# Performance work log

Hardware: AMD Instinct MI355X
Metric: run time of the kernel (lower is better)

The kernel has to match this reference:

```python
import jax, jax.numpy as jnp
import numpy as np
from jax import lax

BS, TLEN, N, S = 256, 3, 90, 65
CHEV, TF, NC = 45, 10, 2
FEAT = (N - 2) * (CHEV - 2)          # 88*43 = 3784
FLAT = TLEN * FEAT                    # 11352
BN_EPS = 1e-5
DN = ('NCHW', 'OIHW', 'NCHW')


def _pearson_cheb_adj(x):
    """x: (B, N, S) -> (B, 3, N, N): [T0=I, T1=L_tilde, T2=2*L*T1-T0 (elementwise)]."""
    xc = x - x.mean(axis=2, keepdims=True)
    y = xc / (jnp.linalg.norm(xc, axis=2, keepdims=True) + 1e-6)
    corr = jnp.einsum('bns,bms->bnm', y, y)
    W = (corr + 1.0) * 0.5
    I = jnp.eye(N, dtype=W.dtype)
    L = I[None] * jnp.sum(W, axis=2)[:, :, None] - W          # D - W, symmetric PSD
    # original uses torch.linalg.eig + .item() (detached); eigvalsh is equivalent for symmetric L
    lam = lax.stop_gradient(jnp.max(jnp.abs(jnp.linalg.eigvalsh(L)), axis=1))
    Lt = 2.0 * L / lam[:, None, None] - I
    T0 = jnp.broadcast_to(I, Lt.shape)
    T2 = 2.0 * Lt * Lt - T0                                   # elementwise, per cheb_polynomial
    return jnp.stack([T0, Lt, T2], axis=1)


def _bn_eval(x, g, b):
    # eval-mode BatchNorm1d with running_mean=0, running_var=1
    return x * (g / jnp.sqrt(jnp.float32(1.0 + BN_EPS))) + b


def setup_inputs() -> dict:
    key = jax.random.key(0)
    ks = jax.random.split(key, 12)
    rn = lambda k, shp, s: jax.random.normal(k, shp, dtype=jnp.float32) * s
    return {
        'fdata':   rn(ks[0], (BS, TLEN, N, S), 1.0),
        'un_w':    rn(ks[1], (N * S, 1), 0.01),
        'un_b':    jnp.zeros((1,), jnp.float32),
        'theta':   rn(ks[2], (3, S, CHEV), 0.05),
        'tconv_w': rn(ks[3], (TF, TLEN, 3, 3), 0.1),
        'tconv_b': jnp.zeros((TF,), jnp.float32),
        'oconv_w': rn(ks[4], (1, TF, 1, 1), 0.1),
        'oconv_b': jnp.zeros((1,), jnp.float32),
        'l1_w':    rn(ks[5], (FLAT, 1024), 0.01),
        'l1_b':    jnp.zeros((1024,), jnp.float32),
        'bn1_g':   jnp.ones((1024,), jnp.float32),
        'bn1_b':   jnp.zeros((1024,), jnp.float32),
        'l2_w':    rn(ks[6], (1024, 256), 0.03),
        'l2_b':    jnp.zeros((256,), jnp.float32),
        'bn2_g':   jnp.ones((256,), jnp.float32),
        'bn2_b':   jnp.zeros((256,), jnp.float32),
        'l3_w':    rn(ks[7], (256, NC), 0.06),
        'l3_b':    jnp.zeros((NC,), jnp.float32),
    }


def reference(fdata, un_w, un_b, theta, tconv_w, tconv_b, oconv_w, oconv_b,
              l1_w, l1_b, bn1_g, bn1_b, l2_w, l2_b, bn2_g, bn2_b, l3_w, l3_b):
    bs, tlen, n, s = fdata.shape
    fp = jnp.transpose(fdata, (1, 0, 2, 3))                    # (tlen, bs, N, S)

    # Uncertainty head (replicates original's tlen-major reshape then bs-major view)
    u = fp.reshape(tlen * bs, n * s) @ un_w + un_b
    cs = jax.nn.sigmoid(u.reshape(bs, tlen, 1))                # (bs, tlen, 1)

    # per-(sample,timestep) pearson Laplacian + Chebyshev basis
    adj = _pearson_cheb_adj(fp.reshape(tlen * bs, n, s))       # (tlen*bs, 3, N, N)
    adj = adj.reshape(tlen, bs, 3, n, n)

    def st_block(adj_t):                                       # adj_t: (bs, 3, N, N)
        h = jax.nn.relu(jnp.einsum('bknm,btms,kso->btno', adj_t, fdata, theta))  # (bs,tlen,N,45)
        c = lax.conv_general_dilated(h, tconv_w, (1, 1), 'VALID', dimension_numbers=DN)
        c = jax.nn.relu(c + tconv_b[None, :, None, None])      # (bs,10,88,43)
        o = lax.conv_general_dilated(c, oconv_w, (1, 1), 'VALID', dimension_numbers=DN)
        return o + oconv_b[None, :, None, None]                # (bs,1,88,43)

    block = jax.vmap(st_block)(adj)                            # (tlen, bs, 1, 88, 43)
    block = block.squeeze(2).reshape(tlen, bs, -1)             # (tlen, bs, 3784)
    block = jnp.transpose(block, (1, 0, 2))                    # (bs, tlen, 3784)

    # sum_s cs[b,s] * block[b,t,f]  ==  block * cs.sum(axis=1) (original broadcast quirk)
    final = block * jnp.sum(cs, axis=1)[:, :, None]            # (bs, tlen, 3784)

    x = final.reshape(bs, -1)                                  # (bs, 11352)
    x = _bn_eval(x @ l1_w + l1_b, bn1_g, bn1_b)
    x = _bn_eval(x @ l2_w + l2_b, bn2_g, bn2_b)
    return jax.nn.softmax(x @ l3_w + l3_b, axis=1)
```

## Files before the change

kernel.cpp:

```cpp
#include <hip/hip_runtime.h>
#include <math.h>

#define TPB 256

constexpr int BSZ = 256, TL = 3, NV = 90, SV = 65, CH = 45;
constexpr int NS = NV*SV;
constexpr int NP = TL*BSZ;
constexpr int NM = NV*NV;
constexpr int CCOL = TL*CH;
constexpr int ZLD = 136;
constexpr int CONV_H = 88, CONV_W = 43, FEAT = CONV_H*CONV_W;
constexpr int FLATD = TL*FEAT;

constexpr size_t OFF_CSUM = 0;
constexpr size_t OFF_LAM  = 256;
constexpr size_t OFF_BEFF = 1024;
constexpr size_t OFF_M    = 1056;
constexpr size_t OFF_MA   = 3104;
constexpr size_t OFF_WEFF = 5152;
constexpr size_t OFF_L    = 32768;
constexpr size_t OFF_Z    = 6291456;
constexpr size_t OFF_X    = 15728640;

__global__ __launch_bounds__(TPB) void k_corr(const float* __restrict__ fdata,
    const float* __restrict__ unw, const float* __restrict__ unb,
    float* __restrict__ Lout, float* __restrict__ csum)
{
    __shared__ float yT[65*96];
    __shared__ float Dl[NV], Wd[NV];
    __shared__ float red[TPB];

    const int q = blockIdx.x, tid = threadIdx.x;
    const int t = q >> 8, b = q & 255;
    const float* xp = fdata + ((size_t)b*TL + t)*NS;
    const int wave = tid >> 6, lane = tid & 63;

    if (tid < NV) Dl[tid] = 0.f;

    float up = 0.f;
    for (int n = wave; n < NV; n += 4) {
        const float* row = xp + n*SV;
        float va = row[lane];
        float vb = (lane == 0) ? row[64] : 0.f;
        up += va*unw[n*SV + lane];
        if (lane == 0) up += vb*unw[n*SV + 64];
        float s1 = va + vb, s2 = va*va + vb*vb;
        #pragma unroll
        for (int o = 1; o < 64; o <<= 1) { s1 += __shfl_xor(s1, o); s2 += __shfl_xor(s2, o); }
        float mean = s1 / SV;
        float var  = s2 - SV*mean*mean;
        float inv  = 1.f / (sqrtf(fmaxf(var, 0.f)) + 1e-6f);
        yT[lane*96 + (((n >> 2) + lane) % 24)*4 + (n & 3)] = (va - mean)*inv;
        if (lane == 0)
            yT[64*96 + (((n >> 2) + 64) % 24)*4 + (n & 3)] = (vb - mean)*inv;
    }
    red[tid] = up; __syncthreads();
    if (tid < 128) red[tid] += red[tid+128]; __syncthreads();
    if (tid < 64)  red[tid] += red[tid+64];  __syncthreads();
    if (tid < 64) {
        float x = red[tid];
        #pragma unroll
        for (int o = 32; o >= 1; o >>= 1) x += __shfl_down(x, o);
        if (tid == 0) {
            float u = x + unb[0];
            atomicAdd(csum + (q/3), 1.f/(1.f + expf(-u)));
        }
    }
    __syncthreads();

    float* Lq = Lout + (size_t)q*NM;
    for (int tile = tid; tile < 529; tile += TPB) {
        int tr = tile / 23, tc = tile - tr*23;
        int n0 = 4*tr, m0 = 4*tc;
        int ca = tr, cb = tc;
        float acc[4][4] = {};
        for (int s = 0; s < SV; ++s) {
            const float* base = &yT[s*96];
            float4 a4 = *(const float4*)(base + 4*ca);
            float4 b4 = *(const float4*)(base + 4*cb);
            float av[4] = {a4.x, a4.y, a4.z, a4.w};
            float bv[4] = {b4.x, b4.y, b4.z, b4.w};
            #pragma unroll
            for (int i = 0; i < 4; ++i)
                #pragma unroll
                for (int j = 0; j < 4; ++j) acc[i][j] += av[i]*bv[j];
            if (++ca == 24) ca = 0;
            if (++cb == 24) cb = 0;
        }
        #pragma unroll
        for (int i = 0; i < 4; ++i) {
            int n = n0 + i;
            if (n >= NV) break;
            float rsum = 0.f;
            #pragma unroll
            for (int j = 0; j < 4; ++j) {
                int m = m0 + j;
                if (m < NV) {
                    float w = (acc[i][j] + 1.f)*0.5f;
                    rsum += w;
                    if (n != m) Lq[n*NV + m] = -w;
                    else        Wd[n] = w;
                }
            }
            atomicAdd(&Dl[n], rsum);
        }
    }
    __syncthreads();
    if (tid < NV) Lq[tid*(NV+1)] = Dl[tid] - Wd[tid];
}

__global__ __launch_bounds__(TPB) void k_eig(const float* __restrict__ L,
                                             float* __restrict__ lamOut)
{
    __shared__ float vbuf[4][2][92];
    const int tid = threadIdx.x, w = tid >> 6, lane = tid & 63;
    const int q = blockIdx.x*4 + w;
    const float* Lq = L + (size_t)q*NM;

    float LA[92], LB[92];
    {
        const float2* ra = (const float2*)(Lq + lane*NV);
        #pragma unroll
        for (int j = 0; j < 45; ++j) { float2 x = ra[j]; LA[2*j] = x.x; LA[2*j+1] = x.y; }
        LA[90] = 0.f; LA[91] = 0.f;
        if (lane < 26) {
            const float2* rb = (const float2*)(Lq + (64 + lane)*NV);
            #pragma unroll
            for (int j = 0; j < 45; ++j) { float2 x = rb[j]; LB[2*j] = x.x; LB[2*j+1] = x.y; }
        } else {
            #pragma unroll
            for (int j = 0; j < 90; ++j) LB[j] = 0.f;
        }
        LB[90] = 0.f; LB[91] = 0.f;
    }
    if (lane < 2) { vbuf[w][0][90+lane] = 0.f; vbuf[w][1][90+lane] = 0.f; }

    float vA = sinf(1.3f*lane + 0.5f) + 0.05f;
    float vB = (lane < 26) ? (sinf(1.3f*(64 + lane) + 0.5f) + 0.05f) : 0.f;
    int cur = 0;
    float wA = 0.f, wB = 0.f;

    auto share = [&]() {
        vbuf[w][cur][lane] = vA;
        if (lane < 26) vbuf[w][cur][64 + lane] = vB;
        __syncthreads();
    };
    auto matvec = [&](float sigma) {
        const float4* v4 = (const float4*)&vbuf[w][cur][0];
        float p0=0.f,p1=0.f,p2=0.f,p3=0.f, r0=0.f,r1=0.f,r2=0.f,r3=0.f;
        #pragma unroll
        for (int j = 0; j < 23; ++j) {
            float4 x = v4[j];
            p0 += LA[4*j]*x.x;   p1 += LA[4*j+1]*x.y;
            p2 += LA[4*j+2]*x.z; p3 += LA[4*j+3]*x.w;
            r0 += LB[4*j]*x.x;   r1 += LB[4*j+1]*x.y;
            r2 += LB[4*j+2]*x.z; r3 += LB[4*j+3]*x.w;
        }
        wA = (p0+p1) + (p2+p3) - sigma*vA;
        wB = (r0+r1) + (r2+r3) - sigma*vB;
        cur ^= 1;
    };
    auto renorm = [&]() {
        float t1 = vA + ((lane < 26) ? vB : 0.f);
        float t2 = vA*vA + ((lane < 26) ? vB*vB : 0.f);
        #pragma unroll
        for (int o = 1; o < 64; o <<= 1) { t1 += __shfl_xor(t1, o); t2 += __shfl_xor(t2, o); }
        float mean = t1*(1.f/90.f);
        float ns   = t2 - 90.f*mean*mean;
        float rn   = rsqrtf(fmaxf(ns, 1e-30f));
        vA = (vA - mean)*rn; vB = (vB - mean)*rn;
    };
    auto dotvw = [&]() {
        float d = vA*wA + ((lane < 26) ? vB*wB : 0.f);
        #pragma unroll
        for (int o = 1; o < 64; o <<= 1) d += __shfl_xor(d, o);
        return d;
    };

    for (int it = 0; it < 8; ++it) { share(); matvec(0.f); vA = wA; vB = wB; }
    renorm();
    share(); matvec(0.f);
    float ray = dotvw();
    float sigma = 0.45f*ray;
    vA = wA - sigma*vA; vB = wB - sigma*vB;
    for (int it = 0; it < 87; ++it) {
        if ((it & 7) == 7) renorm();
        share(); matvec(sigma); vA = wA; vB = wB;
    }
    renorm();
    share(); matvec(0.f);
    float lam = dotvw();
    if (lane == 0) lamOut[q] = lam;
}

__global__ __launch_bounds__(TPB) void k_Z(const float* __restrict__ fdata,
                                           const float* __restrict__ theta,
                                           float* __restrict__ Z)
{
    __shared__ float fl[NV][69];
    __shared__ float thl[3][SV][48];

    const int g = blockIdx.x, tid = threadIdx.x;
    const int b = g/3, tp = g - 3*b;
    const float* fp = fdata + ((size_t)b*TL + tp)*NS;

    for (int idx = tid; idx < NS; idx += TPB) {
        int m = idx / SV, s = idx - m*SV;
        fl[m][s] = fp[idx];
    }
    for (int idx = tid; idx < 3*SV*48; idx += TPB) {
        int k = idx / (SV*48), rr = idx - k*(SV*48);
        int s = rr / 48, o = rr - s*48;
        thl[k][s][o] = (o < CH) ? theta[(k*SV + s)*CH + o] : 0.f;
    }
    __syncthreads();

    for (int tile = tid; tile < 414; tile += TPB) {
        int mt = tile / 18, ct = tile - mt*18;
        int k = ct / 6, ot = ct - 6*k;
        int m0 = 4*mt, o0 = 8*ot;
        float acc[4][8] = {};
        for (int s = 0; s < SV; ++s) {
            float a0 = fl[m0][s], a1 = fl[m0+1][s], a2 = fl[m0+2][s], a3 = fl[m0+3][s];
            float4 t0 = *(const float4*)&thl[k][s][o0];
            float4 t1 = *(const float4*)&thl[k][s][o0+4];
            float tv[8] = {t0.x,t0.y,t0.z,t0.w,t1.x,t1.y,t1.z,t1.w};
            #pragma unroll
            for (int j = 0; j < 8; ++j) {
                acc[0][j] += a0*tv[j]; acc[1][j] += a1*tv[j];
                acc[2][j] += a2*tv[j]; acc[3][j] += a3*tv[j];
            }
        }
        #pragma unroll
        for (int i = 0; i < 4; ++i) {
            int m = m0 + i; if (m >= NV) break;
            float* zp = Z + ((size_t)(k*BSZ + b)*NV + m)*ZLD + tp*CH;
            #pragma unroll
            for (int j = 0; j < 8; ++j) {
                int o = o0 + j;
                if (o < CH) zp[o] = acc[i][j];
            }
        }
    }
    if (tp == 2) {
        for (int idx = tid; idx < 3*NV; idx += TPB) {
            int k = idx / NV, m = idx - k*NV;
            Z[((size_t)(k*BSZ + b)*NV + m)*ZLD + 135] = 0.f;
        }
    }
}

__global__ __launch_bounds__(TPB) void k_hc(const float* __restrict__ L,
    const float* __restrict__ lam, const float* __restrict__ Z,
    const float* __restrict__ tw, const float* __restrict__ tb,
    const float* __restrict__ ow, const float* __restrict__ ob,
    const float* __restrict__ csum, float* __restrict__ X)
{
    __shared__ float smem[12160];
    const int q = blockIdx.x, tid = threadIdx.x;
    const int t = q >> 8, b = q & 255;
    const float il2 = 2.0f / lam[q];

    for (int idx = tid; idx < NM; idx += TPB) {
        int i = idx / NV, j = idx - i*NV;
        smem[i*92 + j] = il2 * L[(size_t)q*NM + idx] - ((i == j) ? 1.f : 0.f);
    }
    __syncthreads();

    float acc[6][8];
    const int tn = tid / 17, tc = tid - tn*17;
    const int n0 = 6*tn, c0 = 8*tc;
    const bool act = (tid < 255);
    if (act) {
        #pragma unroll
        for (int i = 0; i < 6; ++i)
            #pragma unroll
            for (int j = 0; j < 8; ++j) acc[i][j] = 0.f;
        const float* z1p = Z + ((size_t)(BSZ + b)*NV)*ZLD + c0;
        const float* z2p = Z + ((size_t)(2*BSZ + b)*NV)*ZLD + c0;
        for (int m = 0; m < NV; ++m) {
            const float* ar = &smem[m*92 + n0];
            float2 a01 = *(const float2*)(ar);
            float2 a23 = *(const float2*)(ar + 2);
            float2 a45 = *(const float2*)(ar + 4);
            float av[6] = {a01.x, a01.y, a23.x, a23.y, a45.x, a45.y};
            const float4* z1r = (const float4*)(z1p + (size_t)m*ZLD);
            const float4* z2r = (const float4*)(z2p + (size_t)m*ZLD);
            float4 z1a = z1r[0], z1b = z1r[1];
            float4 z2a = z2r[0], z2b = z2r[1];
            float zv1[8] = {z1a.x,z1a.y,z1a.z,z1a.w,z1b.x,z1b.y,z1b.z,z1b.w};
            float zv2[8] = {z2a.x,z2a.y,z2a.z,z2a.w,z2b.x,z2b.y,z2b.z,z2b.w};
            #pragma unroll
            for (int i = 0; i < 6; ++i) {
                float a = av[i], bb = 2.f*a*a;
                #pragma unroll
                for (int j = 0; j < 8; ++j) acc[i][j] += a*zv1[j] + bb*zv2[j];
            }
        }
    }
    __syncthreads();

    float (*hl)[NV][CH] = (float (*)[NV][CH])smem;
    if (act) {
        const float* z0p = Z + ((size_t)b*NV)*ZLD;
        const float* z2p = Z + ((size_t)(2*BSZ + b)*NV)*ZLD;
        #pragma unroll
        for (int i = 0; i < 6; ++i) {
            int n = n0 + i;
            const float4* z0r = (const float4*)(z0p + (size_t)n*ZLD + c0);
            const float4* z2r = (const float4*)(z2p + (size_t)n*ZLD + c0);
            float4 z0a = z0r[0], z0b = z0r[1];
            float4 w2a = z2r[0], w2b = z2r[1];
            float zv0[8] = {z0a.x,z0a.y,z0a.z,z0a.w,z0b.x,z0b.y,z0b.z,z0b.w};
            float zv2[8] = {w2a.x,w2a.y,w2a.z,w2a.w,w2b.x,w2b.y,w2b.z,w2b.w};
            #pragma unroll
            for (int j = 0; j < 8; ++j) {
                int c = c0 + j;
                if (c < CCOL) {
                    float v = fmaxf(acc[i][j] + zv0[j] - zv2[j], 0.f);
                    hl[c/CH][n][c - (c/CH)*CH] = v;
                }
            }
        }
    }
    __syncthreads();

    const float cs  = csum[b];
    const float obv = ob[0];
    float* Xo = X + (size_t)b*FLATD + (size_t)t*FEAT;
    for (int g = tid; g < 88*11; g += TPB) {
        int i = g / 11, jg = g - (g/11)*11, j0 = 4*jg;
        float cf[10][4];
        #pragma unroll
        for (int f = 0; f < 10; ++f) {
            float bv = tb[f];
            cf[f][0] = bv; cf[f][1] = bv; cf[f][2] = bv; cf[f][3] = bv;
        }
        #pragma unroll
        for (int tp = 0; tp < 3; ++tp)
            #pragma unroll
            for (int di = 0; di < 3; ++di) {
                const float* hr = &hl[tp][i + di][j0];
                float w0 = hr[0], w1 = hr[1], w2 = hr[2],
                      w3 = hr[3], w4 = hr[4], w5 = hr[5];
                #pragma unroll
                for (int f = 0; f < 10; ++f) {
                    const float* twp = tw + ((f*TL + tp)*3 + di)*3;
                    float t0 = twp[0], t1 = twp[1], t2 = twp[2];
                    cf[f][0] += w0*t0 + w1*t1 + w2*t2;
                    cf[f][1] += w1*t0 + w2*t1 + w3*t2;
                    cf[f][2] += w2*t0 + w3*t1 + w4*t2;
                    cf[f][3] += w3*t0 + w4*t1 + w5*t2;
                }
            }
        float a0 = 0.f, a1 = 0.f, a2 = 0.f, a3 = 0.f;
        #pragma unroll
        for (int f = 0; f < 10; ++f) {
            float o = ow[f];
            a0 += fmaxf(cf[f][0], 0.f)*o; a1 += fmaxf(cf[f][1], 0.f)*o;
            a2 += fmaxf(cf[f][2], 0.f)*o; a3 += fmaxf(cf[f][3], 0.f)*o;
        }
        int pixb = i*CONV_W + j0;
        Xo[pixb] = (a0 + obv)*cs;
        if (j0 + 1 < CONV_W) Xo[pixb+1] = (a1 + obv)*cs;
        if (j0 + 2 < CONV_W) Xo[pixb+2] = (a2 + obv)*cs;
        if (j0 + 3 < CONV_W) Xo[pixb+3] = (a3 + obv)*cs;
    }
}

__global__ void k_eff1(const float* __restrict__ W2, const float* __restrict__ g2,
                       const float* __restrict__ W3, const float* __restrict__ g1,
                       float* __restrict__ M, float* __restrict__ Ma)
{
    int gid = blockIdx.x*TPB + threadIdx.x;
    if (gid >= 2048) return;
    int i = gid >> 1, c = gid & 1;
    const float rs = rsqrtf(1.f + 1e-5f);
    float acc = 0.f;
    for (int j = 0; j < 256; ++j) acc += W2[i*256 + j]*(g2[j]*rs)*W3[j*2 + c];
    M[gid]  = acc;
    Ma[gid] = acc*(g1[i]*rs);
}

__global__ void k_effb(const float* __restrict__ M, const float* __restrict__ W3,
                       const float* __restrict__ b1, const float* __restrict__ bb1, const float* __restrict__ g1,
                       const float* __restrict__ b2, const float* __restrict__ bb2, const float* __restrict__ g2,
                       const float* __restrict__ b3, float* __restrict__ beff)
{
    __shared__ float r0[TPB], r1[TPB];
    int tid = threadIdx.x;
    const float rs = rsqrtf(1.f + 1e-5f);
    float a0 = 0.f, a1 = 0.f;
    for (int i = tid; i < 1024; i += TPB) {
        float wv = b1[i]*(g1[i]*rs) + bb1[i];
        a0 += wv*M[2*i]; a1 += wv*M[2*i+1];
    }
    for (int j = tid; j < 256; j += TPB) {
        float wv = b2[j]*(g2[j]*rs) + bb2[j];
        a0 += wv*W3[2*j]; a1 += wv*W3[2*j+1];
    }
    r0[tid] = a0; r1[tid] = a1; __syncthreads();
    if (tid < 128) { r0[tid] += r0[tid+128]; r1[tid] += r1[tid+128]; } __syncthreads();
    if (tid < 64)  { r0[tid] += r0[tid+64];  r1[tid] += r1[tid+64];  } __syncthreads();
    if (tid < 64) {
        float x0 = r0[tid], x1 = r1[tid];
        #pragma unroll
        for (int o = 32; o >= 1; o >>= 1) { x0 += __shfl_down(x0, o); x1 += __shfl_down(x1, o); }
        if (tid == 0) { beff[0] = x0 + b3[0]; beff[1] = x1 + b3[1]; }
    }
}

__global__ void k_eff2(const float* __restrict__ W1, const float* __restrict__ Ma,
                       float* __restrict__ Weff)
{
    int tid = threadIdx.x;
    int r = blockIdx.x*4 + (tid >> 6);
    int lane = tid & 63;
    if (r >= FLATD) return;
    const float* wrow = W1 + (size_t)r*1024;
    float a0 = 0.f, a1 = 0.f;
    for (int i = lane; i < 1024; i += 64) {
        float w = wrow[i];
        a0 += w*Ma[2*i]; a1 += w*Ma[2*i+1];
    }
    #pragma unroll
    for (int o = 32; o >= 1; o >>= 1) { a0 += __shfl_down(a0, o); a1 += __shfl_down(a1, o); }
    if (lane == 0) { Weff[2*r] = a0; Weff[2*r+1] = a1; }
}

__global__ void k_logits(const float* __restrict__ x, const float* __restrict__ Weff,
                         const float* __restrict__ beff, float* __restrict__ out)
{
    __shared__ float r0[TPB], r1[TPB];
    int b = blockIdx.x, tid = threadIdx.x;
    const float* xr = x + (size_t)b*FLATD;
    float a0 = 0.f, a1 = 0.f;
    for (int i = tid; i < FLATD; i += TPB) {
        float v = xr[i];
        a0 += v*Weff[2*i]; a1 += v*Weff[2*i+1];
    }
    r0[tid] = a0; r1[tid] = a1; __syncthreads();
    if (tid < 128) { r0[tid] += r0[tid+128]; r1[tid] += r1[tid+128]; } __syncthreads();
    if (tid < 64)  { r0[tid] += r0[tid+64];  r1[tid] += r1[tid+64];  } __syncthreads();
    if (tid < 64) {
        float x0 = r0[tid], x1 = r1[tid];
        #pragma unroll
        for (int o = 32; o >= 1; o >>= 1) { x0 += __shfl_down(x0, o); x1 += __shfl_down(x1, o); }
        if (tid == 0) {
            float l0 = x0 + beff[0], l1 = x1 + beff[1];
            float mx = fmaxf(l0, l1);
            float e0 = expf(l0 - mx), e1 = expf(l1 - mx);
            float s = e0 + e1;
            out[2*b]     = e0/s;
            out[2*b + 1] = e1/s;
        }
    }
}

extern "C" void kernel_launch(void* const* d_in, const int* in_sizes, int n_in,
                              void* d_out, int out_size, void* d_ws, size_t ws_size,
                              hipStream_t stream)
{
    const float* fdata = (const float*)d_in[0];
    const float* un_w  = (const float*)d_in[1];
    const float* un_b  = (const float*)d_in[2];
    const float* theta = (const float*)d_in[3];
    const float* tcw   = (const float*)d_in[4];
    const float* tcb   = (const float*)d_in[5];
    const float* ocw   = (const float*)d_in[6];
    const float* ocb   = (const float*)d_in[7];
    const float* l1w   = (const float*)d_in[8];
    const float* l1b   = (const float*)d_in[9];
    const float* bn1g  = (const float*)d_in[10];
    const float* bn1b  = (const float*)d_in[11];
    const float* l2w   = (const float*)d_in[12];
    const float* l2b   = (const float*)d_in[13];
    const float* bn2g  = (const float*)d_in[14];
    const float* bn2b  = (const float*)d_in[15];
    const float* l3w   = (const float*)d_in[16];
    const float* l3b   = (const float*)d_in[17];

    float* ws   = (float*)d_ws;
    float* csum = ws + OFF_CSUM;
    float* lam  = ws + OFF_LAM;
    float* beff = ws + OFF_BEFF;
    float* M    = ws + OFF_M;
    float* Ma   = ws + OFF_MA;
    float* Weff = ws + OFF_WEFF;
    float* L    = ws + OFF_L;
    float* Z    = ws + OFF_Z;
    float* X    = ws + OFF_X;
    float* out  = (float*)d_out;

    hipMemsetAsync(csum, 0, BSZ*sizeof(float), stream);
    k_corr <<<NP, TPB, 0, stream>>>(fdata, un_w, un_b, L, csum);
    k_eig  <<<NP/4, TPB, 0, stream>>>(L, lam);
    k_Z    <<<BSZ*TL, TPB, 0, stream>>>(fdata, theta, Z);
    k_hc   <<<NP, TPB, 0, stream>>>(L, lam, Z, tcw, tcb, ocw, ocb, csum, X);
    k_eff1 <<<8, TPB, 0, stream>>>(l2w, bn2g, l3w, bn1g, M, Ma);
    k_effb <<<1, TPB, 0, stream>>>(M, l3w, l1b, bn1b, bn1g, l2b, bn2b, bn2g, l3b, beff);
    k_eff2 <<<(FLATD + 3)/4, TPB, 0, stream>>>(l1w, Ma, Weff);
    k_logits<<<BSZ, TPB, 0, stream>>>(X, Weff, beff, out);
}
```

Baseline: 512.5 us.

## Widen k_hc to 512 threads, stage conv weights in LDS, wave-local eig barriers

k_hc now runs with 512 threads per block. Each thread computes 3 rows instead of 6 in the Chebyshev matmul, and the next Z row is prefetched into registers. The conv stage gives each thread an 8-pixel window, uses a padded LDS layout with a row stride of 48, and reads conv weights staged in LDS instead of global memory. In k_eig, block-wide __syncthreads on the per-wave vector buffer is replaced with wave barriers, which cuts synchronisation cost but relies on each wave only touching its own buffer. The changes aim to raise parallelism and reduce redundant global weight reads, at the cost of higher register pressure per thread and a larger LDS footprint.

```diff
diff --git a/kernel.cpp b/kernel.cpp
--- a/kernel.cpp
+++ b/kernel.cpp
@@ -2,6 +2,7 @@
 #include <math.h>
 
 #define TPB 256
+#define TPH 512
 
 constexpr int BSZ = 256, TL = 3, NV = 90, SV = 65, CH = 45;
 constexpr int NS = NV*SV;
@@ -11,6 +12,7 @@
 constexpr int ZLD = 136;
 constexpr int CONV_H = 88, CONV_W = 43, FEAT = CONV_H*CONV_W;
 constexpr int FLATD = TL*FEAT;
+constexpr int HLD = 48;
 
 constexpr size_t OFF_CSUM = 0;
 constexpr size_t OFF_LAM  = 256;
@@ -134,6 +136,7 @@
         LB[90] = 0.f; LB[91] = 0.f;
     }
     if (lane < 2) { vbuf[w][0][90+lane] = 0.f; vbuf[w][1][90+lane] = 0.f; }
+    __builtin_amdgcn_wave_barrier();
 
     float vA = sinf(1.3f*lane + 0.5f) + 0.05f;
     float vB = (lane < 26) ? (sinf(1.3f*(64 + lane) + 0.5f) + 0.05f) : 0.f;
@@ -143,7 +146,7 @@
     auto share = [&]() {
         vbuf[w][cur][lane] = vA;
         if (lane < 26) vbuf[w][cur][64 + lane] = vB;
-        __syncthreads();
+        __builtin_amdgcn_wave_barrier();
     };
     auto matvec = [&](float sigma) {
         const float4* v4 = (const float4*)&vbuf[w][cur][0];
@@ -158,6 +161,7 @@
         }
         wA = (p0+p1) + (p2+p3) - sigma*vA;
         wB = (r0+r1) + (r2+r3) - sigma*vB;
+        __builtin_amdgcn_wave_barrier();
         cur ^= 1;
     };
     auto renorm = [&]() {
@@ -250,48 +254,57 @@
     }
 }
 
-__global__ __launch_bounds__(TPB) void k_hc(const float* __restrict__ L,
+__global__ __launch_bounds__(TPH) void k_hc(const float* __restrict__ L,
     const float* __restrict__ lam, const float* __restrict__ Z,
     const float* __restrict__ tw, const float* __restrict__ tb,
     const float* __restrict__ ow, const float* __restrict__ ob,
     const float* __restrict__ csum, float* __restrict__ X)
 {
-    __shared__ float smem[12160];
+    __shared__ float smem[13344];
+    float* wtl = &smem[12960];
     const int q = blockIdx.x, tid = threadIdx.x;
     const int t = q >> 8, b = q & 255;
     const float il2 = 2.0f / lam[q];
 
-    for (int idx = tid; idx < NM; idx += TPB) {
+    for (int idx = tid; idx < NM; idx += TPH) {
         int i = idx / NV, j = idx - i*NV;
         smem[i*92 + j] = il2 * L[(size_t)q*NM + idx] - ((i == j) ? 1.f : 0.f);
     }
+    if (tid < 270) {
+        int f = tid / 27, r = tid - f*27;
+        int w9 = r / 3, dj = r - 3*w9;
+        wtl[(f*9 + w9)*4 + dj] = tw[tid];
+    } else if (tid < 280) wtl[360 + (tid - 270)] = tb[tid - 270];
+    else if (tid < 290)   wtl[370 + (tid - 280)] = ow[tid - 280];
     __syncthreads();
 
-    float acc[6][8];
+    float acc[3][8];
     const int tn = tid / 17, tc = tid - tn*17;
-    const int n0 = 6*tn, c0 = 8*tc;
-    const bool act = (tid < 255);
+    const int n0 = 3*tn, c0 = 8*tc;
+    const bool act = (tid < 510);
     if (act) {
         #pragma unroll
-        for (int i = 0; i < 6; ++i)
+        for (int i = 0; i < 3; ++i)
             #pragma unroll
             for (int j = 0; j < 8; ++j) acc[i][j] = 0.f;
         const float* z1p = Z + ((size_t)(BSZ + b)*NV)*ZLD + c0;
         const float* z2p = Z + ((size_t)(2*BSZ + b)*NV)*ZLD + c0;
+        float4 nz1a = *(const float4*)(z1p),     nz1b = *(const float4*)(z1p + 4);
+        float4 nz2a = *(const float4*)(z2p),     nz2b = *(const float4*)(z2p + 4);
         for (int m = 0; m < NV; ++m) {
+            float4 z1a = nz1a, z1b = nz1b, z2a = nz2a, z2b = nz2b;
+            if (m < NV-1) {
+                const float* p1 = z1p + (size_t)(m+1)*ZLD;
+                const float* p2 = z2p + (size_t)(m+1)*ZLD;
+                nz1a = *(const float4*)(p1); nz1b = *(const float4*)(p1 + 4);
+                nz2a = *(const float4*)(p2); nz2b = *(const float4*)(p2 + 4);
+            }
             const float* ar = &smem[m*92 + n0];
-            float2 a01 = *(const float2*)(ar);
-            float2 a23 = *(const float2*)(ar + 2);
-            float2 a45 = *(const float2*)(ar + 4);
-            float av[6] = {a01.x, a01.y, a23.x, a23.y, a45.x, a45.y};
-            const float4* z1r = (const float4*)(z1p + (size_t)m*ZLD);
-            const float4* z2r = (const float4*)(z2p + (size_t)m*ZLD);
-            float4 z1a = z1r[0], z1b = z1r[1];
-            float4 z2a = z2r[0], z2b = z2r[1];
+            float av[3] = {ar[0], ar[1], ar[2]};
             float zv1[8] = {z1a.x,z1a.y,z1a.z,z1a.w,z1b.x,z1b.y,z1b.z,z1b.w};
             float zv2[8] = {z2a.x,z2a.y,z2a.z,z2a.w,z2b.x,z2b.y,z2b.z,z2b.w};
             #pragma unroll
-            for (int i = 0; i < 6; ++i) {
+            for (int i = 0; i < 3; ++i) {
                 float a = av[i], bb = 2.f*a*a;
                 #pragma unroll
                 for (int j = 0; j < 8; ++j) acc[i][j] += a*zv1[j] + bb*zv2[j];
@@ -300,12 +313,12 @@
     }
     __syncthreads();
 
-    float (*hl)[NV][CH] = (float (*)[NV][CH])smem;
+    float (*hl)[NV][HLD] = (float (*)[NV][HLD])smem;
     if (act) {
         const float* z0p = Z + ((size_t)b*NV)*ZLD;
         const float* z2p = Z + ((size_t)(2*BSZ + b)*NV)*ZLD;
         #pragma unroll
-        for (int i = 0; i < 6; ++i) {
+        for (int i = 0; i < 3; ++i) {
             int n = n0 + i;
             const float4* z0r = (const float4*)(z0p + (size_t)n*ZLD + c0);
             const float4* z2r = (const float4*)(z2p + (size_t)n*ZLD + c0);
@@ -325,46 +338,47 @@
     }
     __syncthreads();
 
-    const float cs  = csum[b];
-    const float obv = ob[0];
-    float* Xo = X + (size_t)b*FLATD + (size_t)t*FEAT;
-    for (int g = tid; g < 88*11; g += TPB) {
-        int i = g / 11, jg = g - (g/11)*11, j0 = 4*jg;
-        float cf[10][4];
+    if (tid < 528) {
+        const float cs  = csum[b];
+        const float obv = ob[0];
+        float* Xo = X + (size_t)b*FLATD + (size_t)t*FEAT;
+        const int i = tid / 6, jg = tid - (tid/6)*6, j0 = 8*jg;
+        float win[9][12];
+        #pragma unroll
+        for (int tp = 0; tp < 3; ++tp)
+            #pragma unroll
+            for (int di = 0; di < 3; ++di) {
+                const float4* hr = (const float4*)&hl[tp][i + di][j0];
+                float4 ha = hr[0], hb = hr[1], hc4 = hr[2];
+                float* wr = win[tp*3 + di];
+                wr[0]=ha.x; wr[1]=ha.y; wr[2]=ha.z; wr[3]=ha.w;
+                wr[4]=hb.x; wr[5]=hb.y; wr[6]=hb.z; wr[7]=hb.w;
+                wr[8]=hc4.x; wr[9]=hc4.y; wr[10]=hc4.z; wr[11]=hc4.w;
+            }
+        float opix[8] = {};
         #pragma unroll
         for (int f = 0; f < 10; ++f) {
-            float bv = tb[f];
-            cf[f][0] = bv; cf[f][1] = bv; cf[f][2] = bv; cf[f][3] = bv;
-        }
-        #pragma unroll
-        for (int tp = 0; tp < 3; ++tp)
-            #pragma unroll
-            for (int di = 0; di < 3; ++di) {
-                const float* hr = &hl[tp][i + di][j0];
-                float w0 = hr[0], w1 = hr[1], w2 = hr[2],
-                      w3 = hr[3], w4 = hr[4], w5 = hr[5];
+            float c[8];
+            float bv = wtl[360 + f];
+            #pragma unroll
+            for (int px = 0; px < 8; ++px) c[px] = bv;
+            #pragma unroll
+            for (int w9 = 0; w9 < 9; ++w9) {
+                float4 t4 = *(const float4*)&wtl[(f*9 + w9)*4];
+                const float* wr = win[w9];
                 #pragma unroll
-                for (int f = 0; f < 10; ++f) {
-                    const float* twp = tw + ((f*TL + tp)*3 + di)*3;
-                    float t0 = twp[0], t1 = twp[1], t2 = twp[2];
-                    cf[f][0] += w0*t0 + w1*t1 + w2*t2;
-                    cf[f][1] += w1*t0 + w2*t1 + w3*t2;
-                    cf[f][2] += w2*t0 + w3*t1 + w4*t2;
-                    cf[f][3] += w3*t0 + w4*t1 + w5*t2;
-                }
-            }
-        float a0 = 0.f, a1 = 0.f, a2 = 0.f, a3 = 0.f;
-        #pragma unroll
-        for (int f = 0; f < 10; ++f) {
-            float o = ow[f];
-            a0 += fmaxf(cf[f][0], 0.f)*o; a1 += fmaxf(cf[f][1], 0.f)*o;
-            a2 += fmaxf(cf[f][2], 0.f)*o; a3 += fmaxf(cf[f][3], 0.f)*o;
-        }
-        int pixb = i*CONV_W + j0;
-        Xo[pixb] = (a0 + obv)*cs;
-        if (j0 + 1 < CONV_W) Xo[pixb+1] = (a1 + obv)*cs;
-        if (j0 + 2 < CONV_W) Xo[pixb+2] = (a2 + obv)*cs;
-        if (j0 + 3 < CONV_W) Xo[pixb+3] = (a3 + obv)*cs;
+                for (int px = 0; px < 8; ++px)
+                    c[px] += wr[px]*t4.x + wr[px+1]*t4.y + wr[px+2]*t4.z;
+            }
+            float o = wtl[370 + f];
+            #pragma unroll
+            for (int px = 0; px < 8; ++px) opix[px] += fmaxf(c[px], 0.f)*o;
+        }
+        #pragma unroll
+        for (int px = 0; px < 8; ++px) {
+            int j = j0 + px;
+            if (j < CONV_W) Xo[i*CONV_W + j] = (opix[px] + obv)*cs;
+        }
     }
 }
 
@@ -496,7 +510,7 @@
     k_corr <<<NP, TPB, 0, stream>>>(fdata, un_w, un_b, L, csum);
     k_eig  <<<NP/4, TPB, 0, stream>>>(L, lam);
     k_Z    <<<BSZ*TL, TPB, 0, stream>>>(fdata, theta, Z);
-    k_hc   <<<NP, TPB, 0, stream>>>(L, lam, Z, tcw, tcb, ocw, ocb, csum, X);
+    k_hc   <<<NP, TPH, 0, stream>>>(L, lam, Z, tcw, tcb, ocw, ocb, csum, X);
     k_eff1 <<<8, TPB, 0, stream>>>(l2w, bn2g, l3w, bn1g, M, Ma);
     k_effb <<<1, TPB, 0, stream>>>(M, l3w, l1b, bn1b, bn1g, l2b, bn2b, bn2g, l3b, beff);
     k_eff2 <<<(FLATD + 3)/4, TPB, 0, stream>>>(l1w, Ma, Weff);
```

Result: slower. 954.9 us (+86.3%).
